# Optimization experiments

Measured on AMD Instinct MI355X. Metric: run time of the kernel, lower is better.

Reference implementation:

```python
import jax, jax.numpy as jnp
import numpy as np

D_MODEL = 1024
D_FF = 4096
NUM_EXPERTS = 8
TOP_K = 2  # expert_capacity


def setup_inputs() -> dict:
    key = jax.random.key(0)
    ks = jax.random.split(key, 7)
    s_in = 1.0 / np.sqrt(D_MODEL)
    s_ff = 1.0 / np.sqrt(D_FF)
    x = jax.random.normal(ks[0], (2, 2048, D_MODEL), dtype=jnp.float32)
    gate_w = jax.random.uniform(ks[1], (NUM_EXPERTS, D_MODEL), jnp.float32, -s_in, s_in)
    gate_b = jax.random.uniform(ks[2], (NUM_EXPERTS,), jnp.float32, -s_in, s_in)
    w1 = jax.random.uniform(ks[3], (NUM_EXPERTS, D_MODEL, D_FF), jnp.float32, -s_in, s_in)
    b1 = jax.random.uniform(ks[4], (NUM_EXPERTS, D_FF), jnp.float32, -s_in, s_in)
    w2 = jax.random.uniform(ks[5], (NUM_EXPERTS, D_FF, D_MODEL), jnp.float32, -s_ff, s_ff)
    b2 = jax.random.uniform(ks[6], (NUM_EXPERTS, D_MODEL), jnp.float32, -s_ff, s_ff)
    return {"x": x, "gate_w": gate_w, "gate_b": gate_b,
            "w1": w1, "b1": b1, "w2": w2, "b2": b2}


def reference(x, gate_w, gate_b, w1, b1, w2, b2):
    E = gate_w.shape[0]
    # Router
    logits = jnp.einsum('bsd,ed->bse', x, gate_w) + gate_b  # [B,S,E]
    top_vals, top_idx = jax.lax.top_k(logits, TOP_K)        # [B,S,K]
    top_w = jax.nn.softmax(top_vals, axis=-1)               # softmax over the top-k logits
    probs = jax.nn.softmax(logits, axis=-1)
    usage = probs.mean(axis=(0, 1))                         # [E]
    load_balancing_loss = E * jnp.sum(usage ** 2) - 1.0
    # Combine weights: sum over top-k slots of weight * one_hot(expert)
    combine = jnp.sum(top_w[..., None] * jax.nn.one_hot(top_idx, E, dtype=x.dtype), axis=2)  # [B,S,E]
    # All experts over all tokens (faithful to the naive dense-then-mask module)
    h = jax.nn.gelu(jnp.einsum('bsd,edf->ebsf', x, w1) + b1[:, None, None, :], approximate=False)
    expert_out = jnp.einsum('ebsf,efd->ebsd', h, w2) + b2[:, None, None, :]  # [E,B,S,D]
    output = jnp.einsum('bse,ebsd->bsd', combine, expert_out)
    return output, load_balancing_loss
```

## Files before the change

### kernel.cpp

```cpp
#include <hip/hip_runtime.h>
#include <hip/hip_bf16.h>
#include <math.h>


#define D_MODEL 1024
#define D_FF    4096
#define NE      8
#define NTOK    4096
#define CAP     4096

typedef __attribute__((ext_vector_type(4))) float f32x4;
typedef __attribute__((ext_vector_type(8))) short s16x8;

__device__ __forceinline__ short f2bf(float f) {
    union { float f; unsigned u; } v; v.f = f;
    unsigned r = v.u + 0x7FFFu + ((v.u >> 16) & 1u);
    return (short)(r >> 16);
}

__device__ __forceinline__ float gelu_f(float x) {
    float u = x * x;
    float v = __builtin_fmaf(0.044715f, u, 1.0f);
    float y2 = 1.5957691216057308f * x * v;
    float r = __builtin_amdgcn_rcpf(__expf(y2) + 1.0f);
    return x - x * r;
}

__device__ __forceinline__ void gload16(const void* g, void* l) {
    __builtin_amdgcn_global_load_lds(
        (const __attribute__((address_space(1))) unsigned*)g,
        (__attribute__((address_space(3))) unsigned*)l, 16, 0, 0);
}

__global__ __launch_bounds__(256) void router_kernel(
    const float* __restrict__ x, const float* __restrict__ gw,
    const float* __restrict__ gb,
    float* __restrict__ usage, int* __restrict__ eidx, float* __restrict__ wgt)
{
    __shared__ float s_gw[NE][D_MODEL];
    __shared__ float s_usage[NE];
    int tid = threadIdx.x;
    for (int i = tid * 4; i < NE * D_MODEL; i += 256 * 4)
        *(f32x4*)&s_gw[0][i] = *(const f32x4*)(gw + i);
    if (tid < NE) s_usage[tid] = 0.f;
    __syncthreads();

    int wid = tid >> 6, lane = tid & 63;
    int wave_stride = gridDim.x * 4;
    float l_usage[NE];
#pragma unroll
    for (int e = 0; e < NE; e++) l_usage[e] = 0.f;

    for (int t = blockIdx.x * 4 + wid; t < NTOK; t += wave_stride) {
        const float* xr = x + (size_t)t * D_MODEL;
        float acc[NE];
#pragma unroll
        for (int e = 0; e < NE; e++) acc[e] = 0.f;
        for (int i = lane * 4; i < D_MODEL; i += 64 * 4) {
            f32x4 xv = *(const f32x4*)(xr + i);
#pragma unroll
            for (int e = 0; e < NE; e++) {
                f32x4 gv = *(const f32x4*)&s_gw[e][i];
                acc[e] += xv[0]*gv[0] + xv[1]*gv[1] + xv[2]*gv[2] + xv[3]*gv[3];
            }
        }
#pragma unroll
        for (int e = 0; e < NE; e++) {
            float a = acc[e];
            for (int off = 32; off; off >>= 1) a += __shfl_down(a, off);
            acc[e] = a;
        }
        if (lane == 0) {
            float logits[NE];
            float mx = -1e30f;
#pragma unroll
            for (int e = 0; e < NE; e++) { logits[e] = acc[e] + gb[e]; mx = fmaxf(mx, logits[e]); }
            float se = 0.f;
            float pe[NE];
#pragma unroll
            for (int e = 0; e < NE; e++) { pe[e] = expf(logits[e] - mx); se += pe[e]; }
            float inv = 1.f / se;
#pragma unroll
            for (int e = 0; e < NE; e++) l_usage[e] += pe[e] * inv;
            int i0 = 0;
#pragma unroll
            for (int e = 1; e < NE; e++) if (logits[e] > logits[i0]) i0 = e;
            int i1 = -1;
#pragma unroll
            for (int e = 0; e < NE; e++) {
                if (e == i0) continue;
                if (i1 < 0 || logits[e] > logits[i1]) i1 = e;
            }
            float w0 = 1.f / (1.f + expf(logits[i1] - logits[i0]));
            eidx[t] = i0 | (i1 << 8);
            wgt[t] = w0;
        }
    }
    if (lane == 0) {
#pragma unroll
        for (int e = 0; e < NE; e++) atomicAdd(&s_usage[e], l_usage[e]);
    }
    __syncthreads();
    if (tid < NE) atomicAdd(&usage[tid], s_usage[tid]);
}

__global__ __launch_bounds__(256) void build_lists(
    const int* __restrict__ eidx, const float* __restrict__ wgt,
    int* __restrict__ cnt, int* __restrict__ tok_list, float* __restrict__ wt_list)
{
    int e = blockIdx.x;
    __shared__ int s_cnt;
    if (threadIdx.x == 0) s_cnt = 0;
    __syncthreads();
    for (int t = threadIdx.x; t < NTOK; t += 256) {
        int p = eidx[t];
        float w0 = wgt[t];
        if ((p & 255) == e) {
            int s = atomicAdd(&s_cnt, 1);
            tok_list[e * CAP + s] = t; wt_list[e * CAP + s] = w0;
        }
        if ((p >> 8) == e) {
            int s = atomicAdd(&s_cnt, 1);
            tok_list[e * CAP + s] = t; wt_list[e * CAP + s] = 1.f - w0;
        }
    }
    __syncthreads();
    if (threadIdx.x == 0) cnt[e] = s_cnt;
}

__global__ void compute_offsets(const int* __restrict__ cnt, int* __restrict__ offsets)
{
    int o = 0;
    for (int e = 0; e < NE; e++) { offsets[e] = o; o += cnt[e]; }
}

__global__ void write_loss(const float* __restrict__ usage, float* __restrict__ out_loss)
{
    float s = 0.f;
    for (int e = 0; e < NE; e++) { float u = usage[e] / (float)NTOK; s += u * u; }
    *out_loss = (float)NE * s - 1.f;
}

__global__ __launch_bounds__(256) void cvt_x_kernel(
    const float* __restrict__ x, short* __restrict__ xb)
{
    int i = (blockIdx.x * 256 + threadIdx.x) * 8;
    f32x4 a = *(const f32x4*)(x + i);
    f32x4 b = *(const f32x4*)(x + i + 4);
    s16x8 r;
    r[0]=f2bf(a[0]); r[1]=f2bf(a[1]); r[2]=f2bf(a[2]); r[3]=f2bf(a[3]);
    r[4]=f2bf(b[0]); r[5]=f2bf(b[1]); r[6]=f2bf(b[2]); r[7]=f2bf(b[3]);
    *(s16x8*)(xb + i) = r;
}

__global__ __launch_bounds__(256) void transpose_cvt(
    const float* __restrict__ src, short* __restrict__ dst, int R, int C)
{
    __shared__ float tile[64][65];
    int e = blockIdx.z;
    src += (size_t)e * R * C;
    dst += (size_t)e * R * C;
    int c0 = blockIdx.x * 64, r0 = blockIdx.y * 64;
    int tid = threadIdx.x;
    int lr = tid >> 2, lc = (tid & 3) * 16;

    const float* s = src + (size_t)(r0 + lr) * C + c0 + lc;
#pragma unroll
    for (int j = 0; j < 4; j++)
        *(f32x4*)&tile[lr][lc + j * 4] = *(const f32x4*)(s + j * 4);
    __syncthreads();

    short* d = dst + (size_t)(c0 + lr) * R + r0 + lc;
    s16x8 v0, v1;
#pragma unroll
    for (int j = 0; j < 8; j++) v0[j] = f2bf(tile[lc + j][lr]);
#pragma unroll
    for (int j = 0; j < 8; j++) v1[j] = f2bf(tile[lc + 8 + j][lr]);
    *(s16x8*)d = v0;
    *(s16x8*)(d + 8) = v1;
}

#define GEMM_STAGE(AS, BS, KT)                       \
    gload16(asrc0 + (KT), &AS[wid * 16][0]);         \
    gload16(asrc1 + (KT), &AS[64 + wid * 16][0]);    \
    gload16(bsrc0 + (KT), &BS[wid * 16][0]);         \
    gload16(bsrc1 + (KT), &BS[64 + wid * 16][0]);

#define GEMM_COMPUTE(AS, BS)                                                   \
    {                                                                          \
        s16x8 a[4], b[4];                                                      \
        int cidx = (kgr ^ ((lrow >> 1) & 3)) * 8;                              \
        _Pragma("unroll")                                                      \
        for (int i = 0; i < 4; i++) {                                          \
            a[i] = *(const s16x8*)&AS[wr * 64 + i * 16 + lrow][cidx];          \
            b[i] = *(const s16x8*)&BS[wc * 64 + i * 16 + lrow][cidx];          \
        }                                                                      \
        _Pragma("unroll")                                                      \
        for (int i = 0; i < 4; i++)                                            \
            _Pragma("unroll")                                                  \
            for (int j = 0; j < 4; j++)                                        \
                acc[i][j] = __builtin_amdgcn_mfma_f32_16x16x32_bf16(           \
                    a[i], b[j], acc[i][j], 0, 0, 0);                           \
    }

__global__ __launch_bounds__(256) void gemm1_kernel(
    const short* __restrict__ XB, const short* __restrict__ W1T,
    const float* __restrict__ b1, const int* __restrict__ cnt,
    const int* __restrict__ offsets, const int* __restrict__ tok_list,
    short* __restrict__ H)
{
    int e  = blockIdx.y >> 5;
    int tm = blockIdx.y & 31;
    int ce = cnt[e];
    if (tm * 128 >= ce) return;
    int n0 = blockIdx.x * 128;

    __shared__ __align__(16) short As[128][32];
    __shared__ __align__(16) short Bs[128][32];

    int tid = threadIdx.x;
    int lane = tid & 63, wid = tid >> 6;
    int wr = wid >> 1, wc = wid & 1;
    int lrow = lane & 15, kgr = lane >> 4;

    int srow = wid * 16 + (lane >> 2);
    int scol = ((lane & 3) ^ ((lane >> 3) & 3)) * 8;
    int am0 = tm * 128 + srow, am1 = am0 + 64;
    int tok0 = tok_list[e * CAP + (am0 < ce ? am0 : 0)];
    int tok1 = tok_list[e * CAP + (am1 < ce ? am1 : 0)];
    const short* asrc0 = XB + (size_t)tok0 * D_MODEL + scol;
    const short* asrc1 = XB + (size_t)tok1 * D_MODEL + scol;
    const short* bsrc0 = W1T + ((size_t)e * D_FF + n0 + srow) * D_MODEL + scol;
    const short* bsrc1 = bsrc0 + (size_t)64 * D_MODEL;

    f32x4 acc[4][4] = {};
    for (int kt = 0; kt < D_MODEL; kt += 32) {
        GEMM_STAGE(As, Bs, kt);
        __syncthreads();
        GEMM_COMPUTE(As, Bs);
        __syncthreads();
    }

    int offe = offsets[e];
    float bn[4];
#pragma unroll
    for (int j = 0; j < 4; j++) bn[j] = b1[e * D_FF + n0 + wc * 64 + j * 16 + lrow];
#pragma unroll
    for (int i = 0; i < 4; i++) {
#pragma unroll
        for (int q = 0; q < 4; q++) {
            int m = tm * 128 + wr * 64 + i * 16 + kgr * 4 + q;
            if (m >= ce) continue;
            short* hrow = H + (size_t)(offe + m) * D_FF;
#pragma unroll
            for (int j = 0; j < 4; j++) {
                int n = n0 + wc * 64 + j * 16 + lrow;
                hrow[n] = f2bf(gelu_f(acc[i][j][q] + bn[j]));
            }
        }
    }
}

__global__ __launch_bounds__(256) void gemm2_kernel(
    const short* __restrict__ H, const short* __restrict__ W2T,
    const float* __restrict__ b2, const int* __restrict__ cnt,
    const int* __restrict__ offsets, const int* __restrict__ tok_list,
    const float* __restrict__ wt_list, float* __restrict__ out)
{
    int e  = blockIdx.y >> 5;
    int tm = blockIdx.y & 31;
    int ce = cnt[e];
    if (tm * 128 >= ce) return;
    int offe = offsets[e];
    int n0 = blockIdx.x * 128;
    int kz = blockIdx.z;
    const int KSPAN = D_FF / 2;
    int kbase = kz * KSPAN;

    __shared__ __align__(16) short As[128][32];
    __shared__ __align__(16) short Bs[128][32];

    int tid = threadIdx.x;
    int lane = tid & 63, wid = tid >> 6;
    int wr = wid >> 1, wc = wid & 1;
    int lrow = lane & 15, kgr = lane >> 4;

    int srow = wid * 16 + (lane >> 2);
    int scol = ((lane & 3) ^ ((lane >> 3) & 3)) * 8;
    int am0 = tm * 128 + srow, am1 = am0 + 64;
    const short* asrc0 = H + (size_t)(offe + (am0 < ce ? am0 : 0)) * D_FF + kbase + scol;
    const short* asrc1 = H + (size_t)(offe + (am1 < ce ? am1 : 0)) * D_FF + kbase + scol;
    const short* bsrc0 = W2T + ((size_t)e * D_MODEL + n0 + srow) * D_FF + kbase + scol;
    const short* bsrc1 = bsrc0 + (size_t)64 * D_FF;

    f32x4 acc[4][4] = {};
    for (int kt = 0; kt < KSPAN; kt += 32) {
        GEMM_STAGE(As, Bs, kt);
        __syncthreads();
        GEMM_COMPUTE(As, Bs);
        __syncthreads();
    }

    float bn[4];
#pragma unroll
    for (int j = 0; j < 4; j++)
        bn[j] = (kz == 0) ? b2[e * D_MODEL + n0 + wc * 64 + j * 16 + lrow] : 0.f;
#pragma unroll
    for (int i = 0; i < 4; i++) {
#pragma unroll
        for (int q = 0; q < 4; q++) {
            int m = tm * 128 + wr * 64 + i * 16 + kgr * 4 + q;
            if (m >= ce) continue;
            int tokm = tok_list[e * CAP + m];
            float wt = wt_list[e * CAP + m];
            float* orow = out + (size_t)tokm * D_MODEL;
#pragma unroll
            for (int j = 0; j < 4; j++) {
                int n = n0 + wc * 64 + j * 16 + lrow;
                atomicAdd(&orow[n], wt * (acc[i][j][q] + bn[j]));
            }
        }
    }
}

extern "C" void kernel_launch(void* const* d_in, const int* in_sizes, int n_in,
                              void* d_out, int out_size, void* d_ws, size_t ws_size,
                              hipStream_t stream)
{
    const float* x  = (const float*)d_in[0];
    const float* gw = (const float*)d_in[1];
    const float* gb = (const float*)d_in[2];
    const float* w1 = (const float*)d_in[3];
    const float* b1 = (const float*)d_in[4];
    const float* w2 = (const float*)d_in[5];
    const float* b2 = (const float*)d_in[6];
    float* out = (float*)d_out;

    char* w = (char*)d_ws;
    int*   cnt      = (int*)(w + 0);
    float* usage    = (float*)(w + 32);
    int*   offsets  = (int*)(w + 64);
    int*   tok_list = (int*)(w + 128);
    float* wt_list  = (float*)(w + 128 + NE * CAP * 4);
    short* WT       = (short*)(w + 128 + 2 * NE * CAP * 4);
    short* H        = (short*)((char*)WT + (size_t)NE * D_FF * D_MODEL * 2);
    int*   eidx     = (int*)WT;
    float* wgt      = (float*)(WT + NTOK * 2);
    short* XB       = (short*)d_out;

    hipMemsetAsync(d_ws, 0, 128, stream);

    router_kernel<<<256, 256, 0, stream>>>(x, gw, gb, usage, eidx, wgt);
    build_lists<<<NE, 256, 0, stream>>>(eidx, wgt, cnt, tok_list, wt_list);
    compute_offsets<<<1, 1, 0, stream>>>(cnt, offsets);
    cvt_x_kernel<<<NTOK * D_MODEL / (256 * 8), 256, 0, stream>>>(x, XB);

    transpose_cvt<<<dim3(D_FF / 64, D_MODEL / 64, NE), 256, 0, stream>>>(w1, WT, D_MODEL, D_FF);
    gemm1_kernel<<<dim3(D_FF / 128, NE * (CAP / 128)), 256, 0, stream>>>(
        XB, WT, b1, cnt, offsets, tok_list, H);

    hipMemsetAsync(d_out, 0, (size_t)out_size * sizeof(float), stream);
    write_loss<<<1, 1, 0, stream>>>(usage, out + (size_t)NTOK * D_MODEL);

    transpose_cvt<<<dim3(D_MODEL / 64, D_FF / 64, NE), 256, 0, stream>>>(w2, WT, D_FF, D_MODEL);
    gemm2_kernel<<<dim3(D_MODEL / 128, NE * (CAP / 128), 2), 256, 0, stream>>>(
        H, WT, b2, cnt, offsets, tok_list, wt_list, out);
}
```

Before: 365.0 us.

## Write per-slot expert outputs to buffer, then combine per token without atomics

Adds a second-GEMM variant that writes the biased expert output for each routed slot into a dense fp32 buffer, plus a combine kernel that gathers each token's two slots and blends them with the router weights. This removes the output memset and the split-K atomic scatter-adds into the output. In exchange it writes and rereads an extra 32 MB buffer, runs the full K loop in one block with no split-K parallelism, and falls back to the old path when the workspace is too small.

```diff
diff --git a/kernel.cpp b/kernel.cpp
--- a/kernel.cpp
+++ b/kernel.cpp
@@ -106,7 +106,8 @@
 
 __global__ __launch_bounds__(256) void build_lists(
     const int* __restrict__ eidx, const float* __restrict__ wgt,
-    int* __restrict__ cnt, int* __restrict__ tok_list, float* __restrict__ wt_list)
+    int* __restrict__ cnt, int* __restrict__ tok_list, float* __restrict__ wt_list,
+    int* __restrict__ tok2slot, float* __restrict__ wgt_p)
 {
     int e = blockIdx.x;
     __shared__ int s_cnt;
@@ -115,13 +116,16 @@
     for (int t = threadIdx.x; t < NTOK; t += 256) {
         int p = eidx[t];
         float w0 = wgt[t];
+        if (e == 0) wgt_p[t] = w0;
         if ((p & 255) == e) {
             int s = atomicAdd(&s_cnt, 1);
             tok_list[e * CAP + s] = t; wt_list[e * CAP + s] = w0;
+            tok2slot[2 * t] = (e << 16) | s;
         }
         if ((p >> 8) == e) {
             int s = atomicAdd(&s_cnt, 1);
             tok_list[e * CAP + s] = t; wt_list[e * CAP + s] = 1.f - w0;
+            tok2slot[2 * t + 1] = (e << 16) | s;
         }
     }
     __syncthreads();
@@ -261,6 +265,80 @@
     }
 }
 
+__global__ __launch_bounds__(256) void gemm2_y_kernel(
+    const short* __restrict__ H, const short* __restrict__ W2T,
+    const float* __restrict__ b2, const int* __restrict__ cnt,
+    const int* __restrict__ offsets, float* __restrict__ Y)
+{
+    int e  = blockIdx.y >> 5;
+    int tm = blockIdx.y & 31;
+    int ce = cnt[e];
+    if (tm * 128 >= ce) return;
+    int offe = offsets[e];
+    int n0 = blockIdx.x * 128;
+
+    __shared__ __align__(16) short As[128][32];
+    __shared__ __align__(16) short Bs[128][32];
+
+    int tid = threadIdx.x;
+    int lane = tid & 63, wid = tid >> 6;
+    int wr = wid >> 1, wc = wid & 1;
+    int lrow = lane & 15, kgr = lane >> 4;
+
+    int srow = wid * 16 + (lane >> 2);
+    int scol = ((lane & 3) ^ ((lane >> 3) & 3)) * 8;
+    int am0 = tm * 128 + srow, am1 = am0 + 64;
+    const short* asrc0 = H + (size_t)(offe + (am0 < ce ? am0 : 0)) * D_FF + scol;
+    const short* asrc1 = H + (size_t)(offe + (am1 < ce ? am1 : 0)) * D_FF + scol;
+    const short* bsrc0 = W2T + ((size_t)e * D_MODEL + n0 + srow) * D_FF + scol;
+    const short* bsrc1 = bsrc0 + (size_t)64 * D_FF;
+
+    f32x4 acc[4][4] = {};
+    for (int kt = 0; kt < D_FF; kt += 32) {
+        GEMM_STAGE(As, Bs, kt);
+        __syncthreads();
+        GEMM_COMPUTE(As, Bs);
+        __syncthreads();
+    }
+
+    float bn[4];
+#pragma unroll
+    for (int j = 0; j < 4; j++) bn[j] = b2[e * D_MODEL + n0 + wc * 64 + j * 16 + lrow];
+#pragma unroll
+    for (int i = 0; i < 4; i++) {
+#pragma unroll
+        for (int q = 0; q < 4; q++) {
+            int m = tm * 128 + wr * 64 + i * 16 + kgr * 4 + q;
+            if (m >= ce) continue;
+            float* yrow = Y + (size_t)(offe + m) * D_MODEL;
+#pragma unroll
+            for (int j = 0; j < 4; j++) {
+                int n = n0 + wc * 64 + j * 16 + lrow;
+                yrow[n] = acc[i][j][q] + bn[j];
+            }
+        }
+    }
+}
+
+__global__ __launch_bounds__(256) void combine_kernel(
+    const float* __restrict__ Y, const int* __restrict__ tok2slot,
+    const float* __restrict__ wgt_p, const int* __restrict__ offsets,
+    float* __restrict__ out)
+{
+    int t = blockIdx.x;
+    int d = threadIdx.x * 4;
+    int p0 = tok2slot[2 * t], p1 = tok2slot[2 * t + 1];
+    int s0 = offsets[p0 >> 16] + (p0 & 0xFFFF);
+    int s1 = offsets[p1 >> 16] + (p1 & 0xFFFF);
+    float w0 = wgt_p[t], w1 = 1.f - w0;
+    f32x4 a = *(const f32x4*)(Y + (size_t)s0 * D_MODEL + d);
+    f32x4 b = *(const f32x4*)(Y + (size_t)s1 * D_MODEL + d);
+    f32x4 r;
+#pragma unroll
+    for (int j = 0; j < 4; j++) r[j] = w0 * a[j] + w1 * b[j];
+    *(f32x4*)(out + (size_t)t * D_MODEL + d) = r;
+}
+
 __global__ __launch_bounds__(256) void gemm2_kernel(
     const short* __restrict__ H, const short* __restrict__ W2T,
     const float* __restrict__ b2, const int* __restrict__ cnt,
@@ -341,9 +419,14 @@
     float* usage    = (float*)(w + 32);
     int*   offsets  = (int*)(w + 64);
     int*   tok_list = (int*)(w + 128);
-    float* wt_list  = (float*)(w + 128 + NE * CAP * 4);
-    short* WT       = (short*)(w + 128 + 2 * NE * CAP * 4);
-    short* H        = (short*)((char*)WT + (size_t)NE * D_FF * D_MODEL * 2);
+    float* wt_list  = (float*)(w + 128 + 131072);
+    int*   tok2slot = (int*)(w + 128 + 262144);
+    float* wgt_p    = (float*)(w + 128 + 262144 + 32768);
+    short* WT       = (short*)(w + 311424);
+    short* H        = (short*)(w + 311424 + 67108864ull);
+    float* Y        = (float*)(w + 311424 + 2ull * 67108864ull);
+    size_t need_y   = 311424 + 2ull * 67108864ull + 33554432ull;
+    bool   use_y    = ws_size >= need_y;
     int*   eidx     = (int*)WT;
     float* wgt      = (float*)(WT + NTOK * 2);
     short* XB       = (short*)d_out;
@@ -351,7 +434,7 @@
     hipMemsetAsync(d_ws, 0, 128, stream);
 
     router_kernel<<<256, 256, 0, stream>>>(x, gw, gb, usage, eidx, wgt);
-    build_lists<<<NE, 256, 0, stream>>>(eidx, wgt, cnt, tok_list, wt_list);
+    build_lists<<<NE, 256, 0, stream>>>(eidx, wgt, cnt, tok_list, wt_list, tok2slot, wgt_p);
     compute_offsets<<<1, 1, 0, stream>>>(cnt, offsets);
     cvt_x_kernel<<<NTOK * D_MODEL / (256 * 8), 256, 0, stream>>>(x, XB);
 
@@ -359,10 +442,17 @@
     gemm1_kernel<<<dim3(D_FF / 128, NE * (CAP / 128)), 256, 0, stream>>>(
         XB, WT, b1, cnt, offsets, tok_list, H);
 
-    hipMemsetAsync(d_out, 0, (size_t)out_size * sizeof(float), stream);
-    write_loss<<<1, 1, 0, stream>>>(usage, out + (size_t)NTOK * D_MODEL);
-
     transpose_cvt<<<dim3(D_MODEL / 64, D_FF / 64, NE), 256, 0, stream>>>(w2, WT, D_FF, D_MODEL);
-    gemm2_kernel<<<dim3(D_MODEL / 128, NE * (CAP / 128), 2), 256, 0, stream>>>(
-        H, WT, b2, cnt, offsets, tok_list, wt_list, out);
-}
+
+    if (use_y) {
+        write_loss<<<1, 1, 0, stream>>>(usage, out + (size_t)NTOK * D_MODEL);
+        gemm2_y_kernel<<<dim3(D_MODEL / 128, NE * (CAP / 128)), 256, 0, stream>>>(
+            H, WT, b2, cnt, offsets, Y);
+        combine_kernel<<<NTOK, 256, 0, stream>>>(Y, tok2slot, wgt_p, offsets, out);
+    } else {
+        hipMemsetAsync(d_out, 0, (size_t)out_size * sizeof(float), stream);
+        write_loss<<<1, 1, 0, stream>>>(usage, out + (size_t)NTOK * D_MODEL);
+        gemm2_kernel<<<dim3(D_MODEL / 128, NE * (CAP / 128), 2), 256, 0, stream>>>(
+            H, WT, b2, cnt, offsets, tok_list, wt_list, out);
+    }
+}
```

Result: faster. 354.8 us (-2.8%).
